# Performance work log

Hardware: AMD Instinct MI355X
Metric: run time of the kernel (lower is better)

The kernel has to match this reference:

```python
import jax, jax.numpy as jnp
import numpy as np
import math

Q_DIM = 1024
K_DIM = 1024
ATT_DIM = 1024
POS_DIM = 64
B, NQ, NK = 4, 2048, 2048
EPS = 1e-5


def _ln(x, g, b):
    m = jnp.mean(x, axis=-1, keepdims=True)
    v = jnp.var(x, axis=-1, keepdims=True)
    return (x - m) * jax.lax.rsqrt(v + EPS) * g + b


def _sinpos(n, dim):
    # SinPos: exp = 2*arange(dim//2)/dim; pos = p * 10000**-exp; cat(pos, pos+pi/2); sin
    e = 2.0 * jnp.arange(dim // 2, dtype=jnp.float32) / dim      # [dim/2]
    p = jnp.arange(n, dtype=jnp.float32)[:, None]                # [n,1]
    ph = p * jnp.power(10000.0, -e)[None, :]                     # [n,dim/2]
    return jnp.sin(jnp.concatenate([ph, ph + math.pi / 2], axis=1))  # [n,dim]


def setup_inputs() -> dict:
    key = jax.random.key(0)
    ks = jax.random.split(key, 8)
    s = 0.02
    return {
        "q": jax.random.normal(ks[0], (B, NQ, Q_DIM), jnp.float32),
        "k": jax.random.normal(ks[1], (B, NK, K_DIM), jnp.float32),
        "Wq": jax.random.normal(ks[2], (Q_DIM, ATT_DIM), jnp.float32) * s,
        "bq": jnp.zeros((ATT_DIM,), jnp.float32),
        "Wk": jax.random.normal(ks[3], (K_DIM, ATT_DIM), jnp.float32) * s,
        "bk": jnp.zeros((ATT_DIM,), jnp.float32),
        "Wv": jax.random.normal(ks[4], (K_DIM, ATT_DIM), jnp.float32) * s,
        "bv": jnp.zeros((ATT_DIM,), jnp.float32),
        "gq": jnp.ones((ATT_DIM,), jnp.float32), "betaq": jnp.zeros((ATT_DIM,), jnp.float32),
        "gk": jnp.ones((ATT_DIM,), jnp.float32), "betak": jnp.zeros((ATT_DIM,), jnp.float32),
        "gv": jnp.ones((ATT_DIM,), jnp.float32), "betav": jnp.zeros((ATT_DIM,), jnp.float32),
        "Wp": jax.random.normal(ks[5], (POS_DIM, POS_DIM), jnp.float32) * s,
        "bp": jnp.zeros((POS_DIM,), jnp.float32),
    }


def reference(q, k, Wq, bq, Wk, bk, Wv, bv, gq, betaq, gk, betak, gv, betav, Wp, bp):
    qn = _ln(q @ Wq + bq, gq, betaq)          # [B,NQ,D]
    vn = _ln(k @ Wv + bv, gv, betav)          # [B,NK,D]
    kn = _ln(k @ Wk + bk, gk, betak)          # [B,NK,D]
    pos = _sinpos(NK, POS_DIM)                # [NK,P]

    # attention 1: Q=qn, K=kn, V=pos
    s1 = jnp.einsum('bnd,bjd->bnj', qn, kn) * (1.0 / math.sqrt(ATT_DIM))
    a1 = jax.nn.softmax(s1, axis=-1)          # [B,NQ,NK]
    x = jnp.einsum('bnj,jp->bnp', a1, pos)    # [B,NQ,P]

    # pos_net (Linear)
    x = x @ Wp + bp                           # [B,NQ,P]

    # attention 2: Q=x, K=pos, V=vn
    s2 = jnp.einsum('bnp,jp->bnj', x, pos) * (1.0 / math.sqrt(POS_DIM))
    a2 = jax.nn.softmax(s2, axis=-1)          # [B,NQ,NK]
    out = jnp.einsum('bnj,bjd->bnd', a2, vn)  # [B,NQ,D]

    att = jnp.stack([a1, a2], axis=1)         # [B,2,NQ,NK] == torch.cat over head dim
    return out, att
```

## Files before the change

kernel.cpp:

```cpp
#include <hip/hip_runtime.h>
#include <math.h>
#include <stdint.h>


typedef _Float16 f16;
typedef _Float16 f16x4 __attribute__((ext_vector_type(4)));
typedef _Float16 f16x8 __attribute__((ext_vector_type(8)));
typedef float f32x4 __attribute__((ext_vector_type(4)));

static constexpr int CB  = 4;
static constexpr int CNQ = 2048;
static constexpr int CNK = 2048;
static constexpr int CD  = 1024;
static constexpr int CP  = 64;

static __device__ __forceinline__ void async16(const f16* gp, f16* lp) {
  __builtin_amdgcn_global_load_lds(
      (const __attribute__((address_space(1))) void*)(uintptr_t)gp,
      (__attribute__((address_space(3))) void*)(uint32_t)(uintptr_t)lp,
      16, 0, 0);
}

__global__ __launch_bounds__(256) void prep_kernel(
    const float* __restrict__ q, const float* __restrict__ k,
    const float* __restrict__ Wq, const float* __restrict__ Wk,
    const float* __restrict__ Wv,
    f16* __restrict__ q16, f16* __restrict__ k16,
    f16* __restrict__ WqT, f16* __restrict__ WkvT,
    f16* __restrict__ posb, f16* __restrict__ posTb) {
  const int b = blockIdx.x;
  if (b < 512) {
    int tid = b * 256 + threadIdx.x;
    int p = tid >> 11;
    int j = tid & (CNK - 1);
    int i = p & 31;
    float ph = (float)j * powf(10000.0f, -(float)i * (1.0f / 32.0f));
    float v = (p < 32) ? sinf(ph) : cosf(ph);
    posb[j * CP + p]   = (f16)v;
    posTb[p * CNK + j] = (f16)v;
  } else if (b < 512 + 16384) {
    const int NF4 = CB * CNQ * CD / 4;
    int tid = (b - 512) * 256 + threadIdx.x;
    const float* src = (tid < NF4) ? q : k;
    f16* dst = (tid < NF4) ? q16 : k16;
    int i = (tid < NF4) ? tid : tid - NF4;
    float4 v = reinterpret_cast<const float4*>(src)[i];
    f16x4 o = {(f16)v.x, (f16)v.y, (f16)v.z, (f16)v.w};
    reinterpret_cast<f16x4*>(dst)[i] = o;
  } else {
    __shared__ float t[64][65];
    const int idx = b - 16896;
    const int z = idx >> 8;
    const int rem = idx & 255;
    const float* W = (z == 0) ? Wq : (z == 1) ? Wk : Wv;
    f16* WT = (z == 0) ? WqT : (z == 1) ? WkvT : WkvT + 1024 * 1024;
    int k0 = (rem & 15) * 64, n0 = (rem >> 4) * 64;
    int tx = threadIdx.x & 63, ty = threadIdx.x >> 6;
#pragma unroll
    for (int i = 0; i < 16; i++)
      t[ty + 4 * i][tx] = W[(size_t)(k0 + ty + 4 * i) * CD + n0 + tx];
    __syncthreads();
#pragma unroll
    for (int i = 0; i < 16; i++)
      WT[(size_t)(n0 + 4 * i + ty) * CD + k0 + tx] = (f16)t[tx][ty + 4 * i];
  }
}

__global__ __launch_bounds__(256) void transpose_kernel(const f16* __restrict__ in,
                                                        f16* __restrict__ out,
                                                        int ldi) {
  __shared__ f16 t[64][65];
  int n0 = blockIdx.x * 64, d0 = blockIdx.y * 64;
  size_t ibase = (size_t)blockIdx.z * CNK * ldi;
  size_t obase = (size_t)blockIdx.z * CNK * CD;
  int tx = threadIdx.x & 63, ty = threadIdx.x >> 6;
#pragma unroll
  for (int i = 0; i < 16; i++)
    t[ty + 4 * i][tx] = in[ibase + (size_t)(n0 + ty + 4 * i) * ldi + d0 + tx];
  __syncthreads();
#pragma unroll
  for (int i = 0; i < 16; i++)
    out[obase + (size_t)(d0 + ty + 4 * i) * CNK + n0 + tx] = t[tx][ty + 4 * i];
}

template <int BM, int BN>
__device__ __forceinline__ void gemm_core(
    const f16* __restrict__ Ab, const f16* __restrict__ Bb,
    int lda, int ldb, int K, int m0, int n0, f16* sm,
    f32x4 (&acc)[BM / 32][4]) {
  constexpr int FM = BM / 32;
  constexpr int FMC = FM / 2;
  constexpr int TI = (BM + BN) / 64;
  constexpr int bufsz = (BM + BN) * 64;
  const int tid = threadIdx.x;
  const int lane = tid & 63, wid = tid >> 6;
  const int wr = wid >> 2, wc = wid & 3;
  const int lrow = lane & 15, kg = lane >> 4;

  auto stage = [&](int i, int kt, int buf) {
    const int s = i * 512 + tid;
    const int row = s >> 3;
    const int cb = (s & 7) << 4;
    const int scb = cb ^ ((row & 7) << 4);
    const f16* src = (i < BM / 64)
        ? Ab + (size_t)(m0 + row) * lda + kt * 64 + (scb >> 1)
        : Bb + (size_t)(n0 + row - BM) * ldb + kt * 64 + (scb >> 1);
    async16(src, &sm[buf * bufsz + s * 8]);
  };

  const int NTk = K >> 6;
#pragma unroll
  for (int i = 0; i < TI; i++) stage(i, 0, 0);

  for (int t = 0; t < NTk; ++t) {
    const int cur = t & 1;
    if (t + 1 < NTk) {
#pragma unroll
      for (int i = 0; i < TI; i++) stage(i, t + 1, cur ^ 1);
      if constexpr (TI == 8) asm volatile("s_waitcnt vmcnt(8)" ::: "memory");
      else                   asm volatile("s_waitcnt vmcnt(6)" ::: "memory");
    } else {
      asm volatile("s_waitcnt vmcnt(0)" ::: "memory");
    }
    __builtin_amdgcn_s_barrier();

    const f16* smA = sm + cur * bufsz;
    const f16* smB = smA + BM * 64;
    f16x8 bf[2][4];
#pragma unroll
    for (int p = 0; p < 4; ++p) {
      const int kk = p >> 1, mh = p & 1;
      const int Cb = kk * 64 + kg * 16;
      f16x8 af[FMC];
#pragma unroll
      for (int m = 0; m < FMC; ++m) {
        const int ar = wr * (BM / 2) + mh * (FMC * 16) + m * 16 + lrow;
        af[m] = *reinterpret_cast<const f16x8*>(
            &smA[ar * 64 + ((Cb ^ ((ar & 7) << 4)) >> 1)]);
      }
      if (mh == 0) {
#pragma unroll
        for (int n = 0; n < 4; ++n) {
          const int br = wc * 64 + n * 16 + lrow;
          bf[kk][n] = *reinterpret_cast<const f16x8*>(
              &smB[br * 64 + ((Cb ^ ((br & 7) << 4)) >> 1)]);
        }
      }
      __builtin_amdgcn_s_barrier();
      __builtin_amdgcn_s_setprio(1);
#pragma unroll
      for (int m = 0; m < FMC; ++m)
#pragma unroll
        for (int n = 0; n < 4; ++n)
          acc[mh * FMC + m][n] = __builtin_amdgcn_mfma_f32_16x16x32_f16(
              af[m], bf[kk][n], acc[mh * FMC + m][n], 0, 0, 0);
      __builtin_amdgcn_s_setprio(0);
      __builtin_amdgcn_s_barrier();
    }
  }
}

template <int BM, int BN>
__device__ __forceinline__ void epi_f16(
    f32x4 (&acc)[BM / 32][4], f16* sm, f16* Cp, int ldc, int m0, int n0) {
  const int tid = threadIdx.x, lane = tid & 63, wid = tid >> 6;
  const int wr = wid >> 2, wc = wid & 3;
  const int rbase = wr * (BM / 2) + (lane >> 4) * 4;
  const int cbase = wc * 64 + (lane & 15);
  __syncthreads();
#pragma unroll
  for (int mg = 0; mg < BM / 32; mg++)
#pragma unroll
    for (int n = 0; n < 4; n++)
#pragma unroll
      for (int r = 0; r < 4; r++)
        sm[(rbase + mg * 16 + r) * BN + cbase + n * 16] = (f16)acc[mg][n][r];
  __syncthreads();
  constexpr int CH = BM * BN / (512 * 8);
#pragma unroll
  for (int c = 0; c < CH; c++) {
    const int idx = c * 512 + tid;
    const int row = idx / (BN / 8);
    const int cole = (idx % (BN / 8)) * 8;
    f16x8 v = *reinterpret_cast<const f16x8*>(&sm[row * BN + cole]);
    *reinterpret_cast<f16x8*>(Cp + (size_t)(m0 + row) * ldc + n0 + cole) = v;
  }
}

template <int BM, int BN>
__device__ __forceinline__ void epi_exp(
    f32x4 (&acc)[BM / 32][4], f16* sm, float* psum, f16* Cp, int ldc,
    int m0, int n0, float scale, float* PSrow) {
  constexpr int SL = BN / 8;
  const int tid = threadIdx.x, lane = tid & 63, wid = tid >> 6;
  const int wr = wid >> 2, wc = wid & 3;
  const int rbase = wr * (BM / 2) + (lane >> 4) * 4;
  const int cbase = wc * 64 + (lane & 15);
  __syncthreads();
#pragma unroll
  for (int mg = 0; mg < BM / 32; mg++)
#pragma unroll
    for (int n = 0; n < 4; n++)
#pragma unroll
      for (int r = 0; r < 4; r++)
        sm[(rbase + mg * 16 + r) * BN + cbase + n * 16] =
            (f16)__expf(acc[mg][n][r] * scale);
  __syncthreads();
  constexpr int CH = BM * BN / (512 * 8);
#pragma unroll
  for (int c = 0; c < CH; c++) {
    const int idx = c * 512 + tid;
    const int row = idx / SL;
    const int cole = (idx % SL) * 8;
    f16x8 v = *reinterpret_cast<const f16x8*>(&sm[row * BN + cole]);
    *reinterpret_cast<f16x8*>(Cp + (size_t)(m0 + row) * ldc + n0 + cole) = v;
    float p = 0.f;
#pragma unroll
    for (int j = 0; j < 8; j++) p += (float)v[j];
#pragma unroll
    for (int o = 1; o < SL; o <<= 1) p += __shfl_xor(p, o);
    if ((lane & (SL - 1)) == 0) psum[row] = p;
  }
  __syncthreads();
  if (tid < BM) PSrow[tid] = psum[tid];
}

template <int BM, int BN>
__device__ __forceinline__ void epi_f32(
    f32x4 (&acc)[BM / 32][4], f16* smh, float* Cp, int ldc, int m0, int n0) {
  float* st = (float*)smh;
  const int tid = threadIdx.x, lane = tid & 63, wid = tid >> 6;
  const int wr = wid >> 2, wc = wid & 3;
  const int cbase = wc * 64 + (lane & 15);
#pragma unroll
  for (int half = 0; half < 2; half++) {
    __syncthreads();
    if (wr == half) {
#pragma unroll
      for (int mg = 0; mg < BM / 32; mg++)
#pragma unroll
        for (int r = 0; r < 4; r++) {
          const int rloc = (lane >> 4) * 4 + mg * 16 + r;
#pragma unroll
          for (int n = 0; n < 4; n++)
            st[rloc * BN + cbase + n * 16] = acc[mg][n][r];
        }
    }
    __syncthreads();
    constexpr int CH = (BM / 2) * BN / (512 * 4);
#pragma unroll
    for (int c = 0; c < CH; c++) {
      const int idx = c * 512 + tid;
      const int row = idx / (BN / 4);
      const int cole = (idx % (BN / 4)) * 4;
      float4 v = *reinterpret_cast<const float4*>(&st[row * BN + cole]);
      *reinterpret_cast<float4*>(
          Cp + (size_t)(m0 + half * (BM / 2) + row) * ldc + n0 + cole) = v;
    }
  }
}

__global__ __launch_bounds__(512) void gemmIn_kernel(
    const f16* __restrict__ q16, const f16* __restrict__ WqT, f16* __restrict__ tmpq,
    const f16* __restrict__ k16, const f16* __restrict__ WkvT, f16* __restrict__ tmp2) {
  __shared__ __attribute__((aligned(16))) f16 sm[2 * (128 + 256) * 64];
  const int b = blockIdx.x;
  const int swz = (b & 7) * 96 + (b >> 3);
  const f16 *A, *B;
  f16* C;
  int ldc, m0, n0;
  if (swz < 256) {
    const int bx = swz & 63, by = swz >> 6;
    A = q16; B = WqT; C = tmpq; ldc = 1024; m0 = bx * 128; n0 = by * 256;
  } else {
    const int idx = swz - 256;
    const int bx = idx & 63, by = idx >> 6;
    A = k16; B = WkvT; C = tmp2; ldc = 2048; m0 = bx * 128; n0 = by * 256;
  }
  f32x4 acc[4][4] = {};
  gemm_core<128, 256>(A, B, 1024, 1024, 1024, m0, n0, sm, acc);
  epi_f16<128, 256>(acc, sm, C, ldc, m0, n0);
}

__global__ __launch_bounds__(512) void gemmS1_kernel(
    const f16* __restrict__ qn, const f16* __restrict__ kn,
    f16* __restrict__ e1, float* __restrict__ PS) {
  __shared__ __attribute__((aligned(16))) f16 sm[2 * (256 + 256) * 64];
  __shared__ float psum[256];
  const int b = blockIdx.x;
  const int swz = (b & 7) * 32 + (b >> 3);
  const int bz = swz >> 6;
  const int rem = swz & 63;
  const int bx = rem & 7, by = rem >> 3;
  const int m0 = bx * 256, n0 = by * 256;
  const f16* Ab = qn + (size_t)bz * 2048 * 1024;
  const f16* Bb = kn + (size_t)bz * 2048 * 2048;
  f16* Cp = e1 + (size_t)bz * 2048 * 2048;
  f32x4 acc[8][4] = {};
  gemm_core<256, 256>(Ab, Bb, 1024, 2048, 1024, m0, n0, sm, acc);
  epi_exp<256, 256>(acc, sm, psum, Cp, 2048, m0, n0, 0.03125f,
                    PS + (size_t)by * (CB * CNQ) + bz * 2048 + m0);
}

__global__ __launch_bounds__(512) void gemmOut_kernel(
    const f16* __restrict__ e2, const f16* __restrict__ vnT, float* __restrict__ out) {
  __shared__ __attribute__((aligned(16))) f16 sm[2 * (128 + 256) * 64];
  const int b = blockIdx.x;
  const int swz = (b & 7) * 32 + (b >> 3);
  const int bz = swz >> 6;
  const int rem = swz & 63;
  const int bx = rem & 15, by = rem >> 4;
  const int m0 = bx * 128, n0 = by * 256;
  const f16* Ab = e2 + (size_t)bz * 2048 * 2048;
  const f16* Bb = vnT + (size_t)bz * 1024 * 2048;
  float* Cp = out + (size_t)bz * 2048 * 1024;
  f32x4 acc[4][4] = {};
  gemm_core<128, 256>(Ab, Bb, 2048, 2048, 2048, m0, n0, sm, acc);
  epi_f32<128, 256>(acc, sm, Cp, 1024, m0, n0);
}

__global__ __launch_bounds__(256) void ln3_kernel(
    f16* __restrict__ tmpq, f16* __restrict__ tmp2,
    const float* __restrict__ bq, const float* __restrict__ gq, const float* __restrict__ beq,
    const float* __restrict__ bk, const float* __restrict__ gk, const float* __restrict__ bek,
    const float* __restrict__ bv, const float* __restrict__ gv, const float* __restrict__ bev) {
  __shared__ float rs_[4], rq_[4];
  const int z = blockIdx.y;
  f16* rp;
  const float *bias, *g, *beta;
  if (z == 0)      { rp = tmpq + (size_t)blockIdx.x * 1024;        bias = bq; g = gq; beta = beq; }
  else if (z == 1) { rp = tmp2 + (size_t)blockIdx.x * 2048;        bias = bk; g = gk; beta = bek; }
  else             { rp = tmp2 + (size_t)blockIdx.x * 2048 + 1024; bias = bv; g = gv; beta = bev; }
  const int t = threadIdx.x;
  f16x4 v = *reinterpret_cast<const f16x4*>(rp + t * 4);
  float y[4], s = 0.f, q = 0.f;
#pragma unroll
  for (int j = 0; j < 4; j++) {
    y[j] = (float)v[j] + bias[t * 4 + j];
    s += y[j]; q += y[j] * y[j];
  }
#pragma unroll
  for (int o = 32; o; o >>= 1) { s += __shfl_xor(s, o); q += __shfl_xor(q, o); }
  if ((t & 63) == 0) { rs_[t >> 6] = s; rq_[t >> 6] = q; }
  __syncthreads();
  s = rs_[0] + rs_[1] + rs_[2] + rs_[3];
  q = rq_[0] + rq_[1] + rq_[2] + rq_[3];
  const float mean = s * (1.0f / CD);
  const float rstd = rsqrtf(q * (1.0f / CD) - mean * mean + 1e-5f);
  f16x4 o;
#pragma unroll
  for (int j = 0; j < 4; j++) {
    int c = t * 4 + j;
    o[j] = (f16)((y[j] - mean) * rstd * g[c] + beta[c]);
  }
  *reinterpret_cast<f16x4*>(rp + t * 4) = o;
}

__global__ __launch_bounds__(256) void xgemm_kernel(
    const f16* __restrict__ e1, const f16* __restrict__ posTb,
    const float* __restrict__ PS, float* __restrict__ xw, float* __restrict__ att) {
  constexpr int BM = 64, BN = 64;
  __shared__ __attribute__((aligned(16))) f16 As[BM * 32];
  __shared__ __attribute__((aligned(16))) f16 Bs[BN * 32];
  __shared__ float invs[BM];
  const int tid = threadIdx.x;
  const int lane = tid & 63;
  const int wave = tid >> 6;
  const int wr = wave >> 1, wc = wave & 1;
  const int m0 = blockIdx.x * BM;
  const int kbase = blockIdx.z * 1024;
  const int srow = lane >> 2;
  const int scol = (lane & 3) * 8;
  const int lrow = lane & 15;
  const int kg = lane >> 4;

  if (tid < BM) {
    float s = 0.f;
#pragma unroll
    for (int j = 0; j < 8; j++) s += PS[j * (CB * CNQ) + m0 + tid];
    invs[tid] = 1.0f / s;
  }

  const int bb = m0 >> 11, nloc = m0 & (CNQ - 1);
  float* attb = att + ((size_t)(bb << 1) * CNQ + nloc) * CNK + kbase;
  const int arow = tid >> 2, acol = (tid & 3) * 8;

  f32x4 acc[2][2] = {};
  for (int k0 = 0; k0 < 1024; k0 += 32) {
    __syncthreads();
#pragma unroll
    for (int i = wave; i < 8; i += 4) {
      if (i < 4)
        async16(e1 + (size_t)(m0 + i * 16 + srow) * CNK + kbase + k0 + scol, &As[i * 512]);
      else
        async16(posTb + (size_t)((i - 4) * 16 + srow) * CNK + kbase + k0 + scol,
                &Bs[(i - 4) * 512]);
    }
    __syncthreads();
    f16x8 af[2], bfr[2];
#pragma unroll
    for (int m = 0; m < 2; m++)
      af[m] = *reinterpret_cast<const f16x8*>(&As[(wr * 32 + m * 16 + lrow) * 32 + kg * 8]);
#pragma unroll
    for (int n = 0; n < 2; n++)
      bfr[n] = *reinterpret_cast<const f16x8*>(&Bs[(wc * 32 + n * 16 + lrow) * 32 + kg * 8]);
#pragma unroll
    for (int m = 0; m < 2; m++)
#pragma unroll
      for (int n = 0; n < 2; n++)
        acc[m][n] = __builtin_amdgcn_mfma_f32_16x16x32_f16(af[m], bfr[n], acc[m][n], 0, 0, 0);
    {
      const float iv = invs[arow];
      f16x8 v = *reinterpret_cast<const f16x8*>(&As[arow * 32 + acol]);
      float4 w0 = {(float)v[0] * iv, (float)v[1] * iv, (float)v[2] * iv, (float)v[3] * iv};
      float4 w1 = {(float)v[4] * iv, (float)v[5] * iv, (float)v[6] * iv, (float)v[7] * iv};
      float* ap = attb + (size_t)arow * CNK + k0 + acol;
      reinterpret_cast<float4*>(ap)[0] = w0;
      reinterpret_cast<float4*>(ap)[1] = w1;
    }
  }
  float* Cp = xw + (size_t)blockIdx.z * (CB * CNQ) * CP;
  const int crow = m0 + wr * 32 + (lane >> 4) * 4;
  const int ccol = wc * 32 + (lane & 15);
#pragma unroll
  for (int m = 0; m < 2; m++)
#pragma unroll
    for (int n = 0; n < 2; n++)
#pragma unroll
      for (int r = 0; r < 4; r++)
        Cp[(size_t)(crow + m * 16 + r) * CP + ccol + n * 16] = acc[m][n][r];
}

__global__ __launch_bounds__(256) void attn2_kernel(
    const float* __restrict__ xw, const float* __restrict__ Wp,
    const float* __restrict__ bp, const f16* __restrict__ posb,
    const float* __restrict__ PS, f16* __restrict__ e2,
    float* __restrict__ att) {
  __shared__ __attribute__((aligned(16))) f16 shm[32 * 2048 + 32 * 64];
  __shared__ float rsum2[2][32];
  __shared__ float invs[32];
  f16* e2lds = shm;
  f16* xpb = shm + 32 * 2048;
  float* xs = (float*)shm;
  float* Wps = (float*)shm + 32 * 64;
  const int tid = threadIdx.x, l = tid & 63, w = tid >> 6;
  const int r0 = blockIdx.x * 32;
  if (tid < 32) {
    float s = 0.f;
#pragma unroll
    for (int j = 0; j < 8; j++) s += PS[j * (CB * CNQ) + r0 + tid];
    invs[tid] = 1.0f / s;
  }
  __syncthreads();
  if (w < 2) {
#pragma unroll
    for (int i = 0; i < 16; i++) {
      const int row = w * 16 + i;
      const size_t gi = (size_t)(r0 + row) * CP + l;
      xs[row * 64 + l] = (xw[gi] + xw[(size_t)(CB * CNQ) * CP + gi]) * invs[row];
    }
#pragma unroll
    for (int i = w; i < 64; i += 2) Wps[i * 64 + l] = Wp[i * 64 + l];
  }
  const float bpl = bp[l];
  __syncthreads();
  const int rb = (w & 1) * 16, jh = w >> 1;
  if (w < 2) {
#pragma unroll 2
    for (int i = 0; i < 16; i++) {
      float a = bpl;
#pragma unroll 8
      for (int p = 0; p < 64; p++) a = fmaf(xs[(w * 16 + i) * 64 + p], Wps[p * 64 + l], a);
      xpb[(w * 16 + i) * 64 + l] = (f16)a;
    }
  }
  __syncthreads();
  const f16x8 af0 = *reinterpret_cast<const f16x8*>(&xpb[(rb + (l & 15)) * 64 + (l >> 4) * 8]);
  const f16x8 af1 = *reinterpret_cast<const f16x8*>(&xpb[(rb + (l & 15)) * 64 + 32 + (l >> 4) * 8]);
  float rs[4] = {0.f, 0.f, 0.f, 0.f};
  for (int jt = jh * 16; jt < jh * 16 + 16; jt++) {
#pragma unroll
    for (int q4 = 0; q4 < 4; q4++) {
      const int j = jt * 64 + q4 * 16 + (l & 15);
      const f16* pp = posb + (size_t)j * CP + (l >> 4) * 8;
      f16x8 b0 = *reinterpret_cast<const f16x8*>(pp);
      f16x8 b1 = *reinterpret_cast<const f16x8*>(pp + 32);
      f32x4 c = {};
      c = __builtin_amdgcn_mfma_f32_16x16x32_f16(af0, b0, c, 0, 0, 0);
      c = __builtin_amdgcn_mfma_f32_16x16x32_f16(af1, b1, c, 0, 0, 0);
#pragma unroll
      for (int r = 0; r < 4; r++) {
        float ev = __expf(c[r] * 0.125f);
        rs[r] += ev;
        e2lds[(rb + (l >> 4) * 4 + r) * 2048 + j] = (f16)ev;
      }
    }
  }
#pragma unroll
  for (int r = 0; r < 4; r++) {
#pragma unroll
    for (int o = 1; o < 16; o <<= 1) rs[r] += __shfl_xor(rs[r], o);
    if ((l & 15) == 0) rsum2[jh][rb + (l >> 4) * 4 + r] = rs[r];
  }
  __syncthreads();
  const int b = r0 >> 11, nloc = r0 & (CNQ - 1);
  float* attb = att + ((size_t)((b << 1) + 1) * CNQ + nloc) * CNK;
  f16* e2b = e2 + (size_t)r0 * CNK;
  for (int it = 0; it < 16; it++) {
    const int row = it * 2 + (tid >> 7);
    const int col = (tid & 127) * 16;
    const float iv = 1.0f / (rsum2[0][row] + rsum2[1][row]);
    const f16x8 a0 = *reinterpret_cast<const f16x8*>(&e2lds[row * 2048 + col]);
    const f16x8 a1 = *reinterpret_cast<const f16x8*>(&e2lds[row * 2048 + col + 8]);
    float4 w0 = {(float)a0[0] * iv, (float)a0[1] * iv, (float)a0[2] * iv, (float)a0[3] * iv};
    float4 w1 = {(float)a0[4] * iv, (float)a0[5] * iv, (float)a0[6] * iv, (float)a0[7] * iv};
    float4 w2 = {(float)a1[0] * iv, (float)a1[1] * iv, (float)a1[2] * iv, (float)a1[3] * iv};
    float4 w3 = {(float)a1[4] * iv, (float)a1[5] * iv, (float)a1[6] * iv, (float)a1[7] * iv};
    float* ap = attb + (size_t)row * CNK + col;
    reinterpret_cast<float4*>(ap)[0] = w0;
    reinterpret_cast<float4*>(ap)[1] = w1;
    reinterpret_cast<float4*>(ap)[2] = w2;
    reinterpret_cast<float4*>(ap)[3] = w3;
    f16x8 h0 = {(f16)w0.x, (f16)w0.y, (f16)w0.z, (f16)w0.w,
                (f16)w1.x, (f16)w1.y, (f16)w1.z, (f16)w1.w};
    f16x8 h1 = {(f16)w2.x, (f16)w2.y, (f16)w2.z, (f16)w2.w,
                (f16)w3.x, (f16)w3.y, (f16)w3.z, (f16)w3.w};
    f16* ep = e2b + (size_t)row * CNK + col;
    *reinterpret_cast<f16x8*>(ep)     = h0;
    *reinterpret_cast<f16x8*>(ep + 8) = h1;
  }
}

extern "C" void kernel_launch(void* const* d_in, const int* in_sizes, int n_in,
                              void* d_out, int out_size, void* d_ws, size_t ws_size,
                              hipStream_t stream) {
  (void)in_sizes; (void)n_in; (void)out_size; (void)ws_size;
  const float* q    = (const float*)d_in[0];
  const float* k    = (const float*)d_in[1];
  const float* Wq   = (const float*)d_in[2];
  const float* bq   = (const float*)d_in[3];
  const float* Wk   = (const float*)d_in[4];
  const float* bk   = (const float*)d_in[5];
  const float* Wv   = (const float*)d_in[6];
  const float* bv   = (const float*)d_in[7];
  const float* gq   = (const float*)d_in[8];
  const float* betaq= (const float*)d_in[9];
  const float* gk   = (const float*)d_in[10];
  const float* betak= (const float*)d_in[11];
  const float* gv   = (const float*)d_in[12];
  const float* betav= (const float*)d_in[13];
  const float* Wp   = (const float*)d_in[14];
  const float* bp   = (const float*)d_in[15];

  float* out = (float*)d_out;
  float* att = out + (size_t)CB * CNQ * CD;
  char* ws = (char*)d_ws;
  const size_t MB = 1ull << 20;

  f16* q16   = (f16*)(ws);
  f16* k16   = (f16*)(ws + 16 * MB);
  f16* e1    = (f16*)(ws);
  f16* e2    = (f16*)(ws);
  f16* WqT   = (f16*)(ws + 32 * MB);
  f16* WkvT  = (f16*)(ws + 34 * MB);
  f16* posb  = (f16*)(ws + 38 * MB);
  f16* posTb = (f16*)(ws + 38 * MB + 256 * 1024);
  float* xw  = (float*)(ws + 38 * MB + 512 * 1024);
  float* PS  = (float*)(ws + 42 * MB + 512 * 1024);
  f16* tmpq  = (f16*)(ws + 43 * MB);
  f16* tmp2  = (f16*)(ws + 59 * MB);
  f16* vnT   = (f16*)(ws + 91 * MB);
  f16* qn = tmpq;
  f16* kn = tmp2;
  f16* vn = tmp2 + 1024;

  prep_kernel<<<512 + 16384 + 768, 256, 0, stream>>>(
      q, k, Wq, Wk, Wv, q16, k16, WqT, WkvT, posb, posTb);

  gemmIn_kernel<<<768, 512, 0, stream>>>(q16, WqT, tmpq, k16, WkvT, tmp2);
  ln3_kernel<<<dim3(CB * CNQ, 3), 256, 0, stream>>>(
      tmpq, tmp2, bq, gq, betaq, bk, gk, betak, bv, gv, betav);
  transpose_kernel<<<dim3(CNK / 64, CD / 64, CB), 256, 0, stream>>>(vn, vnT, 2048);

  gemmS1_kernel<<<256, 512, 0, stream>>>(qn, kn, e1, PS);

  xgemm_kernel<<<dim3(CB * CNQ / 64, 1, 2), 256, 0, stream>>>(e1, posTb, PS, xw, att);
  attn2_kernel<<<CB * CNQ / 32, 256, 0, stream>>>(xw, Wp, bp, posb, PS, e2, att);

  gemmOut_kernel<<<256, 512, 0, stream>>>(e2, vnT, out);
}
```

Measured before the change: 296.8 us.

## Fuse V layernorm into transpose, simplify GEMM inner loop, widen attn2 blocks

Three independent changes. The GEMM core loop goes from four half-step phases, which split the A fragments in two, to two k-step phases that load all A fragments at once. This means fewer barriers but more registers in use. The V layernorm no longer writes normalized values back. ln3 now only stores the per-token mean and rstd, and the transpose kernel applies the normalization while transposing, which saves one read-modify-write pass over V. attn2 runs 512 threads per block, so four waves share the score columns instead of two and the row sums are combined across four partials.

```diff
diff --git a/kernel.cpp b/kernel.cpp
--- a/kernel.cpp
+++ b/kernel.cpp
@@ -66,30 +66,12 @@
   }
 }
 
-__global__ __launch_bounds__(256) void transpose_kernel(const f16* __restrict__ in,
-                                                        f16* __restrict__ out,
-                                                        int ldi) {
-  __shared__ f16 t[64][65];
-  int n0 = blockIdx.x * 64, d0 = blockIdx.y * 64;
-  size_t ibase = (size_t)blockIdx.z * CNK * ldi;
-  size_t obase = (size_t)blockIdx.z * CNK * CD;
-  int tx = threadIdx.x & 63, ty = threadIdx.x >> 6;
-#pragma unroll
-  for (int i = 0; i < 16; i++)
-    t[ty + 4 * i][tx] = in[ibase + (size_t)(n0 + ty + 4 * i) * ldi + d0 + tx];
-  __syncthreads();
-#pragma unroll
-  for (int i = 0; i < 16; i++)
-    out[obase + (size_t)(d0 + ty + 4 * i) * CNK + n0 + tx] = t[tx][ty + 4 * i];
-}
-
 template <int BM, int BN>
-__device__ __forceinline__ void gemm_core(
+__device__ __forceinline__ void gemm_core2(
     const f16* __restrict__ Ab, const f16* __restrict__ Bb,
     int lda, int ldb, int K, int m0, int n0, f16* sm,
     f32x4 (&acc)[BM / 32][4]) {
   constexpr int FM = BM / 32;
-  constexpr int FMC = FM / 2;
   constexpr int TI = (BM + BN) / 64;
   constexpr int bufsz = (BM + BN) * 64;
   const int tid = threadIdx.x;
@@ -126,34 +108,29 @@
 
     const f16* smA = sm + cur * bufsz;
     const f16* smB = smA + BM * 64;
-    f16x8 bf[2][4];
-#pragma unroll
-    for (int p = 0; p < 4; ++p) {
-      const int kk = p >> 1, mh = p & 1;
+#pragma unroll
+    for (int kk = 0; kk < 2; ++kk) {
       const int Cb = kk * 64 + kg * 16;
-      f16x8 af[FMC];
-#pragma unroll
-      for (int m = 0; m < FMC; ++m) {
-        const int ar = wr * (BM / 2) + mh * (FMC * 16) + m * 16 + lrow;
+      f16x8 af[FM], bf[4];
+#pragma unroll
+      for (int m = 0; m < FM; ++m) {
+        const int ar = wr * (BM / 2) + m * 16 + lrow;
         af[m] = *reinterpret_cast<const f16x8*>(
             &smA[ar * 64 + ((Cb ^ ((ar & 7) << 4)) >> 1)]);
       }
-      if (mh == 0) {
-#pragma unroll
-        for (int n = 0; n < 4; ++n) {
-          const int br = wc * 64 + n * 16 + lrow;
-          bf[kk][n] = *reinterpret_cast<const f16x8*>(
-              &smB[br * 64 + ((Cb ^ ((br & 7) << 4)) >> 1)]);
-        }
+#pragma unroll
+      for (int n = 0; n < 4; ++n) {
+        const int br = wc * 64 + n * 16 + lrow;
+        bf[n] = *reinterpret_cast<const f16x8*>(
+            &smB[br * 64 + ((Cb ^ ((br & 7) << 4)) >> 1)]);
       }
       __builtin_amdgcn_s_barrier();
       __builtin_amdgcn_s_setprio(1);
 #pragma unroll
-      for (int m = 0; m < FMC; ++m)
+      for (int m = 0; m < FM; ++m)
 #pragma unroll
         for (int n = 0; n < 4; ++n)
-          acc[mh * FMC + m][n] = __builtin_amdgcn_mfma_f32_16x16x32_f16(
-              af[m], bf[kk][n], acc[mh * FMC + m][n], 0, 0, 0);
+          acc[m][n] = __builtin_amdgcn_mfma_f32_16x16x32_f16(af[m], bf[n], acc[m][n], 0, 0, 0);
       __builtin_amdgcn_s_setprio(0);
       __builtin_amdgcn_s_barrier();
     }
@@ -278,7 +255,7 @@
     A = k16; B = WkvT; C = tmp2; ldc = 2048; m0 = bx * 128; n0 = by * 256;
   }
   f32x4 acc[4][4] = {};
-  gemm_core<128, 256>(A, B, 1024, 1024, 1024, m0, n0, sm, acc);
+  gemm_core2<128, 256>(A, B, 1024, 1024, 1024, m0, n0, sm, acc);
   epi_f16<128, 256>(acc, sm, C, ldc, m0, n0);
 }
 
@@ -297,7 +274,7 @@
   const f16* Bb = kn + (size_t)bz * 2048 * 2048;
   f16* Cp = e1 + (size_t)bz * 2048 * 2048;
   f32x4 acc[8][4] = {};
-  gemm_core<256, 256>(Ab, Bb, 1024, 2048, 1024, m0, n0, sm, acc);
+  gemm_core2<256, 256>(Ab, Bb, 1024, 2048, 1024, m0, n0, sm, acc);
   epi_exp<256, 256>(acc, sm, psum, Cp, 2048, m0, n0, 0.03125f,
                     PS + (size_t)by * (CB * CNQ) + bz * 2048 + m0);
 }
@@ -315,22 +292,22 @@
   const f16* Bb = vnT + (size_t)bz * 1024 * 2048;
   float* Cp = out + (size_t)bz * 2048 * 1024;
   f32x4 acc[4][4] = {};
-  gemm_core<128, 256>(Ab, Bb, 2048, 2048, 2048, m0, n0, sm, acc);
+  gemm_core2<128, 256>(Ab, Bb, 2048, 2048, 2048, m0, n0, sm, acc);
   epi_f32<128, 256>(acc, sm, Cp, 1024, m0, n0);
 }
 
 __global__ __launch_bounds__(256) void ln3_kernel(
-    f16* __restrict__ tmpq, f16* __restrict__ tmp2,
+    f16* __restrict__ tmpq, f16* __restrict__ tmp2, float* __restrict__ vstat,
     const float* __restrict__ bq, const float* __restrict__ gq, const float* __restrict__ beq,
     const float* __restrict__ bk, const float* __restrict__ gk, const float* __restrict__ bek,
-    const float* __restrict__ bv, const float* __restrict__ gv, const float* __restrict__ bev) {
+    const float* __restrict__ bv) {
   __shared__ float rs_[4], rq_[4];
   const int z = blockIdx.y;
   f16* rp;
   const float *bias, *g, *beta;
   if (z == 0)      { rp = tmpq + (size_t)blockIdx.x * 1024;        bias = bq; g = gq; beta = beq; }
   else if (z == 1) { rp = tmp2 + (size_t)blockIdx.x * 2048;        bias = bk; g = gk; beta = bek; }
-  else             { rp = tmp2 + (size_t)blockIdx.x * 2048 + 1024; bias = bv; g = gv; beta = bev; }
+  else             { rp = tmp2 + (size_t)blockIdx.x * 2048 + 1024; bias = bv; g = nullptr; beta = nullptr; }
   const int t = threadIdx.x;
   f16x4 v = *reinterpret_cast<const f16x4*>(rp + t * 4);
   float y[4], s = 0.f, q = 0.f;
@@ -347,6 +324,10 @@
   q = rq_[0] + rq_[1] + rq_[2] + rq_[3];
   const float mean = s * (1.0f / CD);
   const float rstd = rsqrtf(q * (1.0f / CD) - mean * mean + 1e-5f);
+  if (z == 2) {
+    if (t == 0) { vstat[blockIdx.x] = mean; vstat[CB * CNK + blockIdx.x] = rstd; }
+    return;
+  }
   f16x4 o;
 #pragma unroll
   for (int j = 0; j < 4; j++) {
@@ -354,6 +335,34 @@
     o[j] = (f16)((y[j] - mean) * rstd * g[c] + beta[c]);
   }
   *reinterpret_cast<f16x4*>(rp + t * 4) = o;
+}
+
+__global__ __launch_bounds__(256) void transposeLN_kernel(
+    const f16* __restrict__ tmp2, f16* __restrict__ vnT,
+    const float* __restrict__ vstat, const float* __restrict__ bv,
+    const float* __restrict__ gv, const float* __restrict__ bev) {
+  __shared__ f16 t[64][65];
+  __shared__ float ms[64], rs[64];
+  int n0 = blockIdx.x * 64, d0 = blockIdx.y * 64;
+  size_t ibase = (size_t)blockIdx.z * CNK * 2048;
+  size_t obase = (size_t)blockIdx.z * CNK * CD;
+  int tx = threadIdx.x & 63, ty = threadIdx.x >> 6;
+  const int tokbase = blockIdx.z * CNK + n0;
+  if (threadIdx.x < 64) {
+    ms[threadIdx.x] = vstat[tokbase + threadIdx.x];
+    rs[threadIdx.x] = vstat[CB * CNK + tokbase + threadIdx.x];
+  }
+#pragma unroll
+  for (int i = 0; i < 16; i++)
+    t[ty + 4 * i][tx] = tmp2[ibase + (size_t)(n0 + ty + 4 * i) * 2048 + 1024 + d0 + tx];
+  __syncthreads();
+#pragma unroll
+  for (int i = 0; i < 16; i++) {
+    const int dim = d0 + 4 * i + ty;
+    const float yv = (float)t[tx][ty + 4 * i] + bv[dim];
+    vnT[obase + (size_t)dim * CNK + n0 + tx] =
+        (f16)((yv - ms[tx]) * rs[tx] * gv[dim] + bev[dim]);
+  }
 }
 
 __global__ __launch_bounds__(256) void xgemm_kernel(
@@ -431,13 +440,13 @@
         Cp[(size_t)(crow + m * 16 + r) * CP + ccol + n * 16] = acc[m][n][r];
 }
 
-__global__ __launch_bounds__(256) void attn2_kernel(
+__global__ __launch_bounds__(512) void attn2_kernel(
     const float* __restrict__ xw, const float* __restrict__ Wp,
     const float* __restrict__ bp, const f16* __restrict__ posb,
     const float* __restrict__ PS, f16* __restrict__ e2,
     float* __restrict__ att) {
   __shared__ __attribute__((aligned(16))) f16 shm[32 * 2048 + 32 * 64];
-  __shared__ float rsum2[2][32];
+  __shared__ float rsum4[4][32];
   __shared__ float invs[32];
   f16* e2lds = shm;
   f16* xpb = shm + 32 * 2048;
@@ -464,7 +473,6 @@
   }
   const float bpl = bp[l];
   __syncthreads();
-  const int rb = (w & 1) * 16, jh = w >> 1;
   if (w < 2) {
 #pragma unroll 2
     for (int i = 0; i < 16; i++) {
@@ -475,10 +483,11 @@
     }
   }
   __syncthreads();
+  const int rb = (w & 1) * 16, jh = w >> 1;
   const f16x8 af0 = *reinterpret_cast<const f16x8*>(&xpb[(rb + (l & 15)) * 64 + (l >> 4) * 8]);
   const f16x8 af1 = *reinterpret_cast<const f16x8*>(&xpb[(rb + (l & 15)) * 64 + 32 + (l >> 4) * 8]);
   float rs[4] = {0.f, 0.f, 0.f, 0.f};
-  for (int jt = jh * 16; jt < jh * 16 + 16; jt++) {
+  for (int jt = jh * 8; jt < jh * 8 + 8; jt++) {
 #pragma unroll
     for (int q4 = 0; q4 < 4; q4++) {
       const int j = jt * 64 + q4 * 16 + (l & 15);
@@ -500,16 +509,16 @@
   for (int r = 0; r < 4; r++) {
 #pragma unroll
     for (int o = 1; o < 16; o <<= 1) rs[r] += __shfl_xor(rs[r], o);
-    if ((l & 15) == 0) rsum2[jh][rb + (l >> 4) * 4 + r] = rs[r];
+    if ((l & 15) == 0) rsum4[jh][rb + (l >> 4) * 4 + r] = rs[r];
   }
   __syncthreads();
   const int b = r0 >> 11, nloc = r0 & (CNQ - 1);
   float* attb = att + ((size_t)((b << 1) + 1) * CNQ + nloc) * CNK;
   f16* e2b = e2 + (size_t)r0 * CNK;
-  for (int it = 0; it < 16; it++) {
-    const int row = it * 2 + (tid >> 7);
+  for (int it = 0; it < 8; it++) {
+    const int row = it * 4 + (tid >> 7);
     const int col = (tid & 127) * 16;
-    const float iv = 1.0f / (rsum2[0][row] + rsum2[1][row]);
+    const float iv = 1.0f / (rsum4[0][row] + rsum4[1][row] + rsum4[2][row] + rsum4[3][row]);
     const f16x8 a0 = *reinterpret_cast<const f16x8*>(&e2lds[row * 2048 + col]);
     const f16x8 a1 = *reinterpret_cast<const f16x8*>(&e2lds[row * 2048 + col + 8]);
     float4 w0 = {(float)a0[0] * iv, (float)a0[1] * iv, (float)a0[2] * iv, (float)a0[3] * iv};
@@ -567,25 +576,26 @@
   f16* posTb = (f16*)(ws + 38 * MB + 256 * 1024);
   float* xw  = (float*)(ws + 38 * MB + 512 * 1024);
   float* PS  = (float*)(ws + 42 * MB + 512 * 1024);
+  float* vstat = (float*)(ws + 42 * MB + 768 * 1024);
   f16* tmpq  = (f16*)(ws + 43 * MB);
   f16* tmp2  = (f16*)(ws + 59 * MB);
   f16* vnT   = (f16*)(ws + 91 * MB);
   f16* qn = tmpq;
   f16* kn = tmp2;
-  f16* vn = tmp2 + 1024;
 
   prep_kernel<<<512 + 16384 + 768, 256, 0, stream>>>(
       q, k, Wq, Wk, Wv, q16, k16, WqT, WkvT, posb, posTb);
 
   gemmIn_kernel<<<768, 512, 0, stream>>>(q16, WqT, tmpq, k16, WkvT, tmp2);
   ln3_kernel<<<dim3(CB * CNQ, 3), 256, 0, stream>>>(
-      tmpq, tmp2, bq, gq, betaq, bk, gk, betak, bv, gv, betav);
-  transpose_kernel<<<dim3(CNK / 64, CD / 64, CB), 256, 0, stream>>>(vn, vnT, 2048);
+      tmpq, tmp2, vstat, bq, gq, betaq, bk, gk, betak, bv);
+  transposeLN_kernel<<<dim3(CNK / 64, CD / 64, CB), 256, 0, stream>>>(
+      tmp2, vnT, vstat, bv, gv, betav);
 
   gemmS1_kernel<<<256, 512, 0, stream>>>(qn, kn, e1, PS);
 
   xgemm_kernel<<<dim3(CB * CNQ / 64, 1, 2), 256, 0, stream>>>(e1, posTb, PS, xw, att);
-  attn2_kernel<<<CB * CNQ / 32, 256, 0, stream>>>(xw, Wp, bp, posb, PS, e2, att);
+  attn2_kernel<<<CB * CNQ / 32, 512, 0, stream>>>(xw, Wp, bp, posb, PS, e2, att);
 
   gemmOut_kernel<<<256, 512, 0, stream>>>(e2, vnT, out);
 }
```

Result: no change. 292.5 us (-1.4%).
